# Kernel tuning notes

Measured on AMD Instinct MI355X. Metric: run time of the kernel, lower is better.

Reference implementation:

```python
import jax, jax.numpy as jnp
import numpy as np

TEMPERATURE = 0.07


def setup_inputs() -> dict:
    key = jax.random.key(0)
    k1, k2, k3 = jax.random.split(key, 3)
    B, D = 8192, 256
    projections = jax.random.normal(k1, (B, D), dtype=jnp.float32)
    affordance_ids = jax.random.randint(k2, (B,), 0, 16, dtype=jnp.int64)
    instance_ids = jax.random.randint(k3, (B,), 0, 4096, dtype=jnp.int64)
    return {
        "projections": projections,
        "affordance_ids": affordance_ids,
        "instance_ids": instance_ids,
    }


def reference(projections, affordance_ids, instance_ids):
    B = projections.shape[0]
    # (B, B) similarity logits
    sim = jnp.matmul(projections, projections.T) / TEMPERATURE
    aff_mask = affordance_ids[:, None] == affordance_ids[None, :]
    inst_mask = instance_ids[:, None] == instance_ids[None, :]
    positive_mask = aff_mask & (~inst_mask)
    self_mask = jnp.eye(B, dtype=bool)
    # per-row logsumexp over all j != i (stable, single pass)
    masked_sim = jnp.where(self_mask, -jnp.inf, sim)
    lse = jax.nn.logsumexp(masked_sim, axis=1)  # (B,)
    # loss per positive pair: -sim[i,j] + lse[i]
    per_pair = jnp.where(positive_mask, lse[:, None] - sim, 0.0)
    num_pairs = jnp.sum(positive_mask)
    total = jnp.sum(per_pair)
    return jnp.where(num_pairs > 0, total / num_pairs.astype(sim.dtype), 0.0)
```

## Files before the change

### kernel.cpp

```cpp
#include <hip/hip_runtime.h>
#include <hip/hip_bf16.h>
#include <stdint.h>

#define BN 8192
#define DK 256
#define KLOG2E_T 20.609929155556617f
#define INV_T 14.285714285714286f
#define NEGINF (-3.0e38f)

typedef short vshort8 __attribute__((ext_vector_type(8)));
typedef float vfloat16 __attribute__((ext_vector_type(16)));

__device__ __forceinline__ void gload16(const void* g, void* lds) {
  __builtin_amdgcn_global_load_lds(
      (const __attribute__((address_space(1))) unsigned int*)g,
      (__attribute__((address_space(3))) unsigned int*)lds, 16, 0, 0);
}

__global__ __launch_bounds__(256) void prep_g(
    const float* __restrict__ P, const int* __restrict__ aff,
    const int* __restrict__ inst, ushort* __restrict__ Pb,
    int* __restrict__ keys, int* __restrict__ head, int* __restrict__ nxt,
    int* __restrict__ cntA, float* __restrict__ G) {
  __shared__ float4 Gl[4][16][64];
  __shared__ int hist[16];
  const int t = threadIdx.x;
  const int rg = t >> 6, c = t & 63;
  for (int idx = t; idx < 4096; idx += 256)
    ((float4*)Gl)[idx] = make_float4(0.f, 0.f, 0.f, 0.f);
  if (t < 16) hist[t] = 0;
  __syncthreads();
  const int r0 = blockIdx.x * 64;
  for (int k = 0; k < 16; ++k) {
    const int r = r0 + k * 4 + rg;
    float4 v = ((const float4*)(P + (size_t)r * DK))[c];
    ushort4 h;
    __hip_bfloat16 b;
    b = __float2bfloat16(v.x); h.x = __builtin_bit_cast(unsigned short, b);
    b = __float2bfloat16(v.y); h.y = __builtin_bit_cast(unsigned short, b);
    b = __float2bfloat16(v.z); h.z = __builtin_bit_cast(unsigned short, b);
    b = __float2bfloat16(v.w); h.w = __builtin_bit_cast(unsigned short, b);
    ((ushort4*)(Pb + (size_t)r * DK))[c] = h;
    const int a = aff[r];
    float4 g = Gl[rg][a][c];
    g.x += v.x; g.y += v.y; g.z += v.z; g.w += v.w;
    Gl[rg][a][c] = g;
  }
  if (t < 64) {
    const int g = r0 + t;
    const int a = aff[g];
    const int k = (a << 12) | inst[g];
    keys[g] = k;
    nxt[g] = atomicExch(&head[k], g + 1);
    atomicAdd(&hist[a], 1);
  }
  __syncthreads();
  if (t < 16) atomicAdd(&cntA[t], hist[t]);
  for (int idx = t; idx < 1024; idx += 256) {
    const int a = idx >> 6, cc = idx & 63;
    float4 s0 = Gl[0][a][cc], s1 = Gl[1][a][cc];
    float4 s2 = Gl[2][a][cc], s3 = Gl[3][a][cc];
    atomicAdd(&G[a * 256 + cc * 4 + 0], s0.x + s1.x + s2.x + s3.x);
    atomicAdd(&G[a * 256 + cc * 4 + 1], s0.y + s1.y + s2.y + s3.y);
    atomicAdd(&G[a * 256 + cc * 4 + 2], s0.z + s1.z + s2.z + s3.z);
    atomicAdd(&G[a * 256 + cc * 4 + 3], s0.w + s1.w + s2.w + s3.w);
  }
}

__global__ __launch_bounds__(512, 1) void fused_kernel(
    const ushort* __restrict__ Pb, float2* __restrict__ stats) {
  __shared__ __align__(16) char Ab[2][32768];
  __shared__ __align__(16) char Bb[2][32768];
  __shared__ float2 red[4][256];

  const int tid = threadIdx.x;
  const int w = tid >> 6;
  const int l = tid & 63;
  const int lo = l & 31;
  const int hi = l >> 5;
  const int iw = w >> 2;
  const int jw = w & 3;

  const int bid = blockIdx.x;
  const int xcd = bid & 7;
  const int inner = (bid >> 3) & 3;
  const int it = bid >> 5;
  const int jc = xcd * 4 + inner;
  const int ibase = it * 256;
  const int jcbase = jc * 256;

  const int srow = tid >> 3;
  const int sswz = ((tid & 7) ^ (srow & 7) ^ (5 * ((srow >> 3) & 1))) * 16;
  const char* gA = (const char*)(Pb + (size_t)ibase * DK);
  const char* gB = (const char*)(Pb + (size_t)jcbase * DK);

#define STAGE(kt1, bsel)                                                       \
  {                                                                            \
    const int ko = (kt1) * 128;                                                \
    _Pragma("unroll") for (int e = 0; e < 4; ++e) {                            \
      gload16(gA + (size_t)(srow + 64 * e) * 512 + ko + sswz,                  \
              Ab[bsel] + e * 8192 + tid * 16);                                 \
      gload16(gB + (size_t)(srow + 64 * e) * 512 + ko + sswz,                  \
              Bb[bsel] + e * 8192 + tid * 16);                                 \
    }                                                                          \
  }
#define BARRIER asm volatile("s_barrier" ::: "memory")
#define DRAIN_BARRIER asm volatile("s_waitcnt vmcnt(0)\ns_barrier" ::: "memory")

  const int rswz = (lo & 7) ^ (5 * ((lo >> 3) & 1));
  int swzk[4];
#pragma unroll
  for (int kk = 0; kk < 4; ++kk) swzk[kk] = ((kk * 2 + hi) ^ rswz) * 16;
  const int rowAb0 = (iw * 128 + lo) * 128;
  const int rowBb0 = (jw * 64 + lo) * 128;

  vfloat16 acc[4][2];
#pragma unroll
  for (int mi = 0; mi < 4; ++mi)
#pragma unroll
    for (int nj = 0; nj < 2; ++nj)
#pragma unroll
      for (int r = 0; r < 16; ++r) acc[mi][nj][r] = 0.f;

  STAGE(0, 0);
  DRAIN_BARRIER;

  for (int kt = 0; kt < 4; ++kt) {
    const int s = kt & 1;
    if (kt < 3) STAGE(kt + 1, s ^ 1);
    const char* As = Ab[s];
    const char* Bs = Bb[s];

    vshort8 bf[2][4], af[2][4];
#pragma unroll
    for (int nj = 0; nj < 2; ++nj)
#pragma unroll
      for (int kk = 0; kk < 4; ++kk)
        bf[nj][kk] = *(const vshort8*)(Bs + rowBb0 + nj * 4096 + swzk[kk]);
#pragma unroll
    for (int mi = 0; mi < 2; ++mi)
#pragma unroll
      for (int kk = 0; kk < 4; ++kk)
        af[mi][kk] = *(const vshort8*)(As + rowAb0 + mi * 4096 + swzk[kk]);
    __builtin_amdgcn_s_setprio(1);
#pragma unroll
    for (int kk = 0; kk < 4; ++kk)
#pragma unroll
      for (int mi = 0; mi < 2; ++mi) {
        acc[mi][0] = __builtin_amdgcn_mfma_f32_32x32x16_bf16(bf[0][kk], af[mi][kk], acc[mi][0], 0, 0, 0);
        acc[mi][1] = __builtin_amdgcn_mfma_f32_32x32x16_bf16(bf[1][kk], af[mi][kk], acc[mi][1], 0, 0, 0);
      }
    __builtin_amdgcn_s_setprio(0);
    BARRIER;

#pragma unroll
    for (int mi = 0; mi < 2; ++mi)
#pragma unroll
      for (int kk = 0; kk < 4; ++kk)
        af[mi][kk] = *(const vshort8*)(As + rowAb0 + (mi + 2) * 4096 + swzk[kk]);
    __builtin_amdgcn_s_setprio(1);
#pragma unroll
    for (int kk = 0; kk < 4; ++kk)
#pragma unroll
      for (int mi = 0; mi < 2; ++mi) {
        acc[mi + 2][0] = __builtin_amdgcn_mfma_f32_32x32x16_bf16(bf[0][kk], af[mi][kk], acc[mi + 2][0], 0, 0, 0);
        acc[mi + 2][1] = __builtin_amdgcn_mfma_f32_32x32x16_bf16(bf[1][kk], af[mi][kk], acc[mi + 2][1], 0, 0, 0);
      }
    __builtin_amdgcn_s_setprio(0);
    DRAIN_BARRIER;
  }

#pragma unroll
  for (int mi = 0; mi < 4; ++mi) {
    const int gib = ibase + iw * 128 + mi * 32;
#pragma unroll
    for (int nj = 0; nj < 2; ++nj) {
      if (gib == (jcbase + jw * 64 + nj * 32)) {
#pragma unroll
        for (int r = 0; r < 16; ++r) {
          const int jj = (r & 3) + 8 * (r >> 2) + 4 * hi;
          if (jj == lo) acc[mi][nj][r] = NEGINF;
        }
      }
    }
  }
#pragma unroll
  for (int mi = 0; mi < 4; ++mi) {
    float mx = NEGINF;
#pragma unroll
    for (int nj = 0; nj < 2; ++nj)
#pragma unroll
      for (int r = 0; r < 16; ++r) mx = fmaxf(mx, acc[mi][nj][r]);
    mx = fmaxf(mx, __shfl_xor(mx, 32));
    const float rc = -mx * KLOG2E_T;
    float sv = 0.f;
#pragma unroll
    for (int nj = 0; nj < 2; ++nj)
#pragma unroll
      for (int r = 0; r < 16; ++r)
        sv += exp2f(fmaf(acc[mi][nj][r], KLOG2E_T, rc));
    sv += __shfl_xor(sv, 32);
    if (hi == 0) red[jw][iw * 128 + mi * 32 + lo] = make_float2(mx, sv);
  }
  __syncthreads();
  if (tid < 256) {
    float2 a = red[0][tid];
    float mm = a.x, ss = a.y;
#pragma unroll
    for (int j2 = 1; j2 < 4; ++j2) {
      float2 b = red[j2][tid];
      float M = fmaxf(mm, b.x);
      ss = ss * exp2f((mm - M) * KLOG2E_T) + b.y * exp2f((b.x - M) * KLOG2E_T);
      mm = M;
    }
    stats[(size_t)jc * BN + ibase + tid] = make_float2(mm, ss);
  }
#undef STAGE
#undef BARRIER
#undef DRAIN_BARRIER
}

__global__ __launch_bounds__(256) void final_rows(
    const float2* __restrict__ stats, const float* __restrict__ P,
    const float* __restrict__ G, const int* __restrict__ keys,
    const int* __restrict__ head, const int* __restrict__ nxt,
    const int* __restrict__ cntA, float2* __restrict__ part) {
  const int t = threadIdx.x;
  const int rloc = t >> 6;
  const int lane = t & 63;
  const int i = blockIdx.x * 4 + rloc;

  float2 st = stats[(size_t)(lane & 31) * BN + i];
  float mm = st.x, ss = st.y;
#pragma unroll
  for (int off = 1; off < 32; off <<= 1) {
    float mo = __shfl_xor(mm, off);
    float so = __shfl_xor(ss, off);
    float M = fmaxf(mm, mo);
    ss = ss * exp2f((mm - M) * KLOG2E_T) + so * exp2f((mo - M) * KLOG2E_T);
    mm = M;
  }
  const float lse = logf(ss) + mm * INV_T;

  const int key = keys[i];
  const int a = key >> 12;
  float4 p4 = ((const float4*)(P + (size_t)i * 256))[lane];
  float4 g4 = ((const float4*)(G + a * 256))[lane];
  float acc = p4.x * g4.x + p4.y * g4.y + p4.z * g4.z + p4.w * g4.w;
  int cnt = 0;
  int j = head[key];
  while (j > 0) {
    const int jr = j - 1;
    float4 q4 = ((const float4*)(P + (size_t)jr * 256))[lane];
    acc -= p4.x * q4.x + p4.y * q4.y + p4.z * q4.z + p4.w * q4.w;
    cnt++;
    j = nxt[jr];
  }
#pragma unroll
  for (int off = 1; off < 64; off <<= 1) acc += __shfl_xor(acc, off);
  const float pc = (float)(cntA[a] - cnt);
  const float contrib = pc * lse - acc * INV_T;

  __shared__ float cs[4], ps[4];
  if (lane == 0) { cs[rloc] = contrib; ps[rloc] = pc; }
  __syncthreads();
  if (t == 0)
    part[blockIdx.x] = make_float2(cs[0] + cs[1] + cs[2] + cs[3],
                                   ps[0] + ps[1] + ps[2] + ps[3]);
}

__global__ void finalize(const float2* __restrict__ part, float* __restrict__ out) {
  const int t = threadIdx.x;
  float c = 0.f, p = 0.f;
  for (int k = t; k < 2048; k += 256) {
    float2 v = part[k];
    c += v.x;
    p += v.y;
  }
#pragma unroll
  for (int off = 1; off < 64; off <<= 1) {
    c += __shfl_xor(c, off);
    p += __shfl_xor(p, off);
  }
  __shared__ float cs[4], ps[4];
  if ((t & 63) == 0) { cs[t >> 6] = c; ps[t >> 6] = p; }
  __syncthreads();
  if (t == 0) {
    c = cs[0] + cs[1] + cs[2] + cs[3];
    p = ps[0] + ps[1] + ps[2] + ps[3];
    out[0] = (p > 0.f) ? (c / p) : 0.f;
  }
}

extern "C" void kernel_launch(void* const* d_in, const int* in_sizes, int n_in,
                              void* d_out, int out_size, void* d_ws, size_t ws_size,
                              hipStream_t stream) {
  const float* P = (const float*)d_in[0];
  const int* aff = (const int*)d_in[1];
  const int* inst = (const int*)d_in[2];
  char* ws = (char*)d_ws;
  ushort* Pb    = (ushort*)(ws);
  int*    keys  = (int*)(ws + 4194304);
  int*    nxt   = (int*)(ws + 4227072);
  int*    head  = (int*)(ws + 4259840);
  float*  G     = (float*)(ws + 4521984);
  int*    cntA  = (int*)(ws + 4538368);
  float2* stats = (float2*)(ws + 4538496);
  float2* part  = (float2*)(ws + 6635648);
  float* out = (float*)d_out;

  hipMemsetAsync(head, 0, 278592, stream);
  prep_g<<<128, 256, 0, stream>>>(P, aff, inst, Pb, keys, head, nxt, cntA, G);
  fused_kernel<<<1024, 512, 0, stream>>>(Pb, stats);
  final_rows<<<2048, 256, 0, stream>>>(stats, P, G, keys, head, nxt, cntA, part);
  finalize<<<1, 256, 0, stream>>>(part, out);
}
```

Measured before the change: 89.67 us.

## Deepen GEMM K-pipeline to 4-stage ring and shrink hash table head array

The GEMM main loop changes from two 128-wide K stages with double buffering to eight 64-wide K phases in a 4-slot LDS ring. Loads run three phases ahead, and vmcnt-based waits replace the full drain barriers. Separately, the instance hash table head array is shrunk 8x by bucketing keys with k>>3. The chain walk now checks keys[jr]==key to filter collisions, which allows a much smaller memset. The cost is longer collision chains with extra key loads in final_rows.

Measured after the change: 102.4 us. 1.14x slower.

```diff
diff --git a/kernel.cpp b/kernel.cpp
--- a/kernel.cpp
+++ b/kernel.cpp
@@ -51,7 +51,7 @@
     const int a = aff[g];
     const int k = (a << 12) | inst[g];
     keys[g] = k;
-    nxt[g] = atomicExch(&head[k], g + 1);
+    nxt[g] = atomicExch(&head[k >> 3], g + 1);
     atomicAdd(&hist[a], 1);
   }
   __syncthreads();
@@ -69,8 +69,8 @@
 
 __global__ __launch_bounds__(512, 1) void fused_kernel(
     const ushort* __restrict__ Pb, float2* __restrict__ stats) {
-  __shared__ __align__(16) char Ab[2][32768];
-  __shared__ __align__(16) char Bb[2][32768];
+  __shared__ __align__(16) char Ab[4 * 16384];
+  __shared__ __align__(16) char Bb[4 * 16384];
   __shared__ float2 red[4][256];
 
   const int tid = threadIdx.x;
@@ -89,86 +89,76 @@
   const int ibase = it * 256;
   const int jcbase = jc * 256;
 
-  const int srow = tid >> 3;
-  const int sswz = ((tid & 7) ^ (srow & 7) ^ (5 * ((srow >> 3) & 1))) * 16;
+  const int srow0 = tid >> 2;
+  const int sstg = ((tid & 3) ^ (srow0 & 3)) * 16;
   const char* gA = (const char*)(Pb + (size_t)ibase * DK);
   const char* gB = (const char*)(Pb + (size_t)jcbase * DK);
 
-#define STAGE(kt1, bsel)                                                       \
+#define STAGE_STEP(P)                                                          \
   {                                                                            \
-    const int ko = (kt1) * 128;                                                \
-    _Pragma("unroll") for (int e = 0; e < 4; ++e) {                            \
-      gload16(gA + (size_t)(srow + 64 * e) * 512 + ko + sswz,                  \
-              Ab[bsel] + e * 8192 + tid * 16);                                 \
-      gload16(gB + (size_t)(srow + 64 * e) * 512 + ko + sswz,                  \
-              Bb[bsel] + e * 8192 + tid * 16);                                 \
+    const int ko = (P) * 64;                                                   \
+    char* Ad = Ab + ((P) & 3) * 16384 + tid * 16;                              \
+    char* Bd = Bb + ((P) & 3) * 16384 + tid * 16;                              \
+    gload16(gA + (size_t)srow0 * 512 + ko + sstg, Ad);                         \
+    gload16(gA + (size_t)(srow0 + 128) * 512 + ko + sstg, Ad + 8192);          \
+    gload16(gB + (size_t)srow0 * 512 + ko + sstg, Bd);                         \
+    gload16(gB + (size_t)(srow0 + 128) * 512 + ko + sstg, Bd + 8192);          \
+  }
+
+  const int rowAb0 = (iw * 128 + lo) * 64;
+  const int rowBb0 = (jw * 64 + lo) * 64;
+  int swzk[2];
+#pragma unroll
+  for (int kk = 0; kk < 2; ++kk) swzk[kk] = ((kk * 2 + hi) ^ (lo & 3)) * 16;
+
+  vfloat16 acc[4][2];
+#pragma unroll
+  for (int mi = 0; mi < 4; ++mi)
+#pragma unroll
+    for (int nj = 0; nj < 2; ++nj)
+#pragma unroll
+      for (int r = 0; r < 16; ++r) acc[mi][nj][r] = 0.f;
+
+#define PHASE(P, VMC)                                                          \
+  {                                                                            \
+    asm volatile("s_waitcnt vmcnt(" #VMC ")" ::: "memory");                    \
+    __builtin_amdgcn_s_barrier();                                              \
+    const char* As = Ab + ((P) & 3) * 16384;                                   \
+    const char* Bs = Bb + ((P) & 3) * 16384;                                   \
+    vshort8 bf[2][2], af[4][2];                                                \
+    _Pragma("unroll") for (int kk = 0; kk < 2; ++kk) {                         \
+      _Pragma("unroll") for (int nj = 0; nj < 2; ++nj)                         \
+        bf[nj][kk] = *(const vshort8*)(Bs + rowBb0 + nj * 2048 + swzk[kk]);    \
+      _Pragma("unroll") for (int mi = 0; mi < 4; ++mi)                         \
+        af[mi][kk] = *(const vshort8*)(As + rowAb0 + mi * 2048 + swzk[kk]);    \
     }                                                                          \
-  }
-#define BARRIER asm volatile("s_barrier" ::: "memory")
-#define DRAIN_BARRIER asm volatile("s_waitcnt vmcnt(0)\ns_barrier" ::: "memory")
-
-  const int rswz = (lo & 7) ^ (5 * ((lo >> 3) & 1));
-  int swzk[4];
-#pragma unroll
-  for (int kk = 0; kk < 4; ++kk) swzk[kk] = ((kk * 2 + hi) ^ rswz) * 16;
-  const int rowAb0 = (iw * 128 + lo) * 128;
-  const int rowBb0 = (jw * 64 + lo) * 128;
-
-  vfloat16 acc[4][2];
-#pragma unroll
-  for (int mi = 0; mi < 4; ++mi)
-#pragma unroll
-    for (int nj = 0; nj < 2; ++nj)
-#pragma unroll
-      for (int r = 0; r < 16; ++r) acc[mi][nj][r] = 0.f;
-
-  STAGE(0, 0);
-  DRAIN_BARRIER;
-
-  for (int kt = 0; kt < 4; ++kt) {
-    const int s = kt & 1;
-    if (kt < 3) STAGE(kt + 1, s ^ 1);
-    const char* As = Ab[s];
-    const char* Bs = Bb[s];
-
-    vshort8 bf[2][4], af[2][4];
-#pragma unroll
-    for (int nj = 0; nj < 2; ++nj)
-#pragma unroll
-      for (int kk = 0; kk < 4; ++kk)
-        bf[nj][kk] = *(const vshort8*)(Bs + rowBb0 + nj * 4096 + swzk[kk]);
-#pragma unroll
-    for (int mi = 0; mi < 2; ++mi)
-#pragma unroll
-      for (int kk = 0; kk < 4; ++kk)
-        af[mi][kk] = *(const vshort8*)(As + rowAb0 + mi * 4096 + swzk[kk]);
-    __builtin_amdgcn_s_setprio(1);
-#pragma unroll
-    for (int kk = 0; kk < 4; ++kk)
-#pragma unroll
-      for (int mi = 0; mi < 2; ++mi) {
-        acc[mi][0] = __builtin_amdgcn_mfma_f32_32x32x16_bf16(bf[0][kk], af[mi][kk], acc[mi][0], 0, 0, 0);
-        acc[mi][1] = __builtin_amdgcn_mfma_f32_32x32x16_bf16(bf[1][kk], af[mi][kk], acc[mi][1], 0, 0, 0);
-      }
-    __builtin_amdgcn_s_setprio(0);
-    BARRIER;
-
-#pragma unroll
-    for (int mi = 0; mi < 2; ++mi)
-#pragma unroll
-      for (int kk = 0; kk < 4; ++kk)
-        af[mi][kk] = *(const vshort8*)(As + rowAb0 + (mi + 2) * 4096 + swzk[kk]);
-    __builtin_amdgcn_s_setprio(1);
-#pragma unroll
-    for (int kk = 0; kk < 4; ++kk)
-#pragma unroll
-      for (int mi = 0; mi < 2; ++mi) {
-        acc[mi + 2][0] = __builtin_amdgcn_mfma_f32_32x32x16_bf16(bf[0][kk], af[mi][kk], acc[mi + 2][0], 0, 0, 0);
-        acc[mi + 2][1] = __builtin_amdgcn_mfma_f32_32x32x16_bf16(bf[1][kk], af[mi][kk], acc[mi + 2][1], 0, 0, 0);
-      }
-    __builtin_amdgcn_s_setprio(0);
-    DRAIN_BARRIER;
-  }
+    if ((P) + 3 < 8) STAGE_STEP((P) + 3);                                      \
+    asm volatile("s_waitcnt lgkmcnt(0)" ::: "memory");                         \
+    __builtin_amdgcn_sched_barrier(0);                                         \
+    __builtin_amdgcn_s_setprio(1);                                             \
+    _Pragma("unroll") for (int kk = 0; kk < 2; ++kk)                           \
+      _Pragma("unroll") for (int mi = 0; mi < 4; ++mi) {                       \
+        acc[mi][0] = __builtin_amdgcn_mfma_f32_32x32x16_bf16(                  \
+            bf[0][kk], af[mi][kk], acc[mi][0], 0, 0, 0);                       \
+        acc[mi][1] = __builtin_amdgcn_mfma_f32_32x32x16_bf16(                  \
+            bf[1][kk], af[mi][kk], acc[mi][1], 0, 0, 0);                       \
+      }                                                                        \
+    __builtin_amdgcn_s_setprio(0);                                             \
+    __builtin_amdgcn_s_barrier();                                              \
+  }
+
+  STAGE_STEP(0);
+  STAGE_STEP(1);
+  STAGE_STEP(2);
+
+  PHASE(0, 8)
+  PHASE(1, 8)
+  PHASE(2, 8)
+  PHASE(3, 8)
+  PHASE(4, 8)
+  PHASE(5, 8)
+  PHASE(6, 4)
+  PHASE(7, 0)
 
 #pragma unroll
   for (int mi = 0; mi < 4; ++mi) {
@@ -215,9 +205,8 @@
     }
     stats[(size_t)jc * BN + ibase + tid] = make_float2(mm, ss);
   }
-#undef STAGE
-#undef BARRIER
-#undef DRAIN_BARRIER
+#undef STAGE_STEP
+#undef PHASE
 }
 
 __global__ __launch_bounds__(256) void final_rows(
@@ -248,12 +237,14 @@
   float4 g4 = ((const float4*)(G + a * 256))[lane];
   float acc = p4.x * g4.x + p4.y * g4.y + p4.z * g4.z + p4.w * g4.w;
   int cnt = 0;
-  int j = head[key];
+  int j = head[key >> 3];
   while (j > 0) {
     const int jr = j - 1;
-    float4 q4 = ((const float4*)(P + (size_t)jr * 256))[lane];
-    acc -= p4.x * q4.x + p4.y * q4.y + p4.z * q4.z + p4.w * q4.w;
-    cnt++;
+    if (keys[jr] == key) {
+      float4 q4 = ((const float4*)(P + (size_t)jr * 256))[lane];
+      acc -= p4.x * q4.x + p4.y * q4.y + p4.z * q4.z + p4.w * q4.w;
+      cnt++;
+    }
     j = nxt[jr];
   }
 #pragma unroll
@@ -303,13 +294,13 @@
   int*    keys  = (int*)(ws + 4194304);
   int*    nxt   = (int*)(ws + 4227072);
   int*    head  = (int*)(ws + 4259840);
-  float*  G     = (float*)(ws + 4521984);
-  int*    cntA  = (int*)(ws + 4538368);
-  float2* stats = (float2*)(ws + 4538496);
-  float2* part  = (float2*)(ws + 6635648);
+  float*  G     = (float*)(ws + 4292608);
+  int*    cntA  = (int*)(ws + 4308992);
+  float2* stats = (float2*)(ws + 4309056);
+  float2* part  = (float2*)(ws + 6406208);
   float* out = (float*)d_out;
 
-  hipMemsetAsync(head, 0, 278592, stream);
+  hipMemsetAsync(head, 0, 49216, stream);
   prep_g<<<128, 256, 0, stream>>>(P, aff, inst, Pb, keys, head, nxt, cntA, G);
   fused_kernel<<<1024, 512, 0, stream>>>(Pb, stats);
   final_rows<<<2048, 256, 0, stream>>>(stats, P, G, keys, head, nxt, cntA, part);
```
